# Performance work log

Hardware: AMD Instinct MI355X
Metric: run time of the kernel (lower is better)

Reference implementation:

```python
import jax, jax.numpy as jnp
import numpy as np

BLOCK_Q = 64
BLOCK_KV = 64
TOPK_RATIO = 0.125


def setup_inputs() -> dict:
    key = jax.random.key(0)
    k1, k2, k3 = jax.random.split(key, 3)
    B, H, L, D = 1, 16, 8192, 64
    q = jax.random.normal(k1, (B, H, L, D), dtype=jnp.float32)
    k = jax.random.normal(k2, (B, H, L, D), dtype=jnp.float32)
    v = jax.random.normal(k3, (B, H, L, D), dtype=jnp.float32)
    return {"q": q, "k": k, "v": v}


def _sparse_lut(q, k):
    # get_sparse_map: block mean-pool q and mean-centered k, score blocks, top-k key blocks
    B, H, L, D = q.shape
    Mb, Nb = L // BLOCK_Q, L // BLOCK_KV
    q_pool = q.reshape(B, H, Mb, BLOCK_Q, D).mean(axis=3)          # [B,H,Mb,D]
    smooth_k = k - k.mean(axis=-2, keepdims=True)
    k_pool = smooth_k.reshape(B, H, Nb, BLOCK_KV, D).mean(axis=3)  # [B,H,Nb,D]
    pred = jnp.einsum('bhmd,bhnd->bhmn', q_pool, k_pool)           # [B,H,Mb,Nb]
    topk = int(TOPK_RATIO * Nb)
    _, lut = jax.lax.top_k(pred, topk)                             # [B,H,Mb,topk]
    return lut


def reference(q, k, v):
    B, H, L, D = q.shape
    Mb, Nb = L // BLOCK_Q, L // BLOCK_KV
    lut = _sparse_lut(q, k)                                        # [B,H,Mb,T] int32
    T = lut.shape[-1]
    sm_scale = D ** -0.5

    kb = k.reshape(B, H, Nb, BLOCK_KV, D)
    vb = v.reshape(B, H, Nb, BLOCK_KV, D)
    bi = jnp.arange(B)[:, None, None, None]
    hi = jnp.arange(H)[None, :, None, None]
    # gather selected KV blocks per query block: [B,H,Mb,T,BLOCK_KV,D]
    k_sel = kb[bi, hi, lut].reshape(B, H, Mb, T * BLOCK_KV, D)
    v_sel = vb[bi, hi, lut].reshape(B, H, Mb, T * BLOCK_KV, D)

    qb = q.reshape(B, H, Mb, BLOCK_Q, D)
    s = jnp.einsum('bhmqd,bhmkd->bhmqk', qb, k_sel) * sm_scale     # [B,H,Mb,BQ,T*BKV]
    p = jax.nn.softmax(s, axis=-1)
    o = jnp.einsum('bhmqk,bhmkd->bhmqd', p, v_sel)
    return o.reshape(B, H, L, D)
```

## Files before the change

### kernel.cpp

```cpp
#include <hip/hip_runtime.h>
#include <hip/hip_bf16.h>


#define H_  16
#define L_  8192
#define D_  64
#define MB_ 128
#define NB_ 128
#define TK_ 16
#define ST_ 72

typedef __bf16 bf16x8 __attribute__((ext_vector_type(8)));
typedef __bf16 bf16x4 __attribute__((ext_vector_type(4)));
typedef short  s16x4  __attribute__((ext_vector_type(4)));
typedef float  f32x4  __attribute__((ext_vector_type(4)));
typedef unsigned short u16x8 __attribute__((ext_vector_type(8)));

union BFU { __hip_bfloat16 h; unsigned short u; };

static __device__ inline unsigned short f2bfu(float f) {
  BFU c; c.h = __float2bfloat16(f); return c.u;
}

static __device__ inline f32x4 mfma16(bf16x4 a, bf16x4 b, f32x4 c) {
#if __has_builtin(__builtin_amdgcn_mfma_f32_16x16x16bf16_1k)
  return __builtin_amdgcn_mfma_f32_16x16x16bf16_1k(
      __builtin_bit_cast(s16x4, a), __builtin_bit_cast(s16x4, b), c, 0, 0, 0);
#elif __has_builtin(__builtin_amdgcn_mfma_f32_16x16x16_bf16)
  return __builtin_amdgcn_mfma_f32_16x16x16_bf16(a, b, c, 0, 0, 0);
#else
  f32x4 d = c;
  asm("v_mfma_f32_16x16x16_bf16 %0, %1, %2, %0" : "+v"(d) : "v"(a), "v"(b));
  return d;
#endif
}

static __device__ inline bf16x4 lo4(bf16x8 v) {
  return __builtin_shufflevector(v, v, 0, 1, 2, 3);
}
static __device__ inline bf16x4 hi4(bf16x8 v) {
  return __builtin_shufflevector(v, v, 4, 5, 6, 7);
}

__device__ unsigned short g_qb[(size_t)H_ * L_ * D_];
__device__ unsigned short g_kf[(size_t)H_ * NB_ * 4096];
__device__ unsigned short g_vf[(size_t)H_ * NB_ * 4096];
__device__ float g_qpool[H_ * NB_ * 64];
__device__ float g_kpool[H_ * NB_ * 64];
__device__ int   g_lut[H_ * MB_ * TK_];

static __device__ inline void cvt8_2(const float4& f0, const float4& f1,
                                     unsigned short* dst) {
  u16x8 s;
  s[0] = f2bfu(f0.x); s[1] = f2bfu(f0.y); s[2] = f2bfu(f0.z); s[3] = f2bfu(f0.w);
  s[4] = f2bfu(f1.x); s[5] = f2bfu(f1.y); s[6] = f2bfu(f1.z); s[7] = f2bfu(f1.w);
  *(u16x8*)dst = s;
}

static __device__ inline void cvt8_2s(const float4& f0, const float4& f1,
                                      unsigned short* dst, float sc) {
  u16x8 s;
  s[0] = f2bfu(f0.x * sc); s[1] = f2bfu(f0.y * sc);
  s[2] = f2bfu(f0.z * sc); s[3] = f2bfu(f0.w * sc);
  s[4] = f2bfu(f1.x * sc); s[5] = f2bfu(f1.y * sc);
  s[6] = f2bfu(f1.z * sc); s[7] = f2bfu(f1.w * sc);
  *(u16x8*)dst = s;
}

__global__ __launch_bounds__(256)
void fusedpool_kernel(const float* __restrict__ q,
                      const float* __restrict__ k,
                      const float* __restrict__ v) {
  __shared__ float qt[64 * 64];
  __shared__ float kt[64 * 64];
  __shared__ __align__(16) unsigned short vt_s[64 * ST_];
  __shared__ float pq[4][64], pk[4][64];

  const int b = blockIdx.x;
  const int t = threadIdx.x;
  const int r = t >> 2, c = (t & 3) * 16;
  const size_t base = (size_t)b * 4096 + r * 64 + c;
  const float cs = 0.18033688011112042f;

  float4 qf0 = *(const float4*)(q + base),      qf1 = *(const float4*)(q + base + 4);
  float4 qf2 = *(const float4*)(q + base + 8),  qf3 = *(const float4*)(q + base + 12);
  float4 kf0 = *(const float4*)(k + base),      kf1 = *(const float4*)(k + base + 4);
  float4 kf2 = *(const float4*)(k + base + 8),  kf3 = *(const float4*)(k + base + 12);
  float4 vf0 = *(const float4*)(v + base),      vf1 = *(const float4*)(v + base + 4);
  float4 vf2 = *(const float4*)(v + base + 8),  vf3 = *(const float4*)(v + base + 12);

  cvt8_2s(qf0, qf1, g_qb + base, cs);  cvt8_2s(qf2, qf3, g_qb + base + 8, cs);

  {
    const int w_k = r >> 4, l16k = r & 15;
    const int hf = c >> 5, quadA = (c & 31) >> 3;
    unsigned short* kfp = g_kf + ((size_t)b * 4 + w_k) * 1024 + hf * 512 + l16k * 8;
    cvt8_2(kf0, kf1, kfp + quadA * 128);
    cvt8_2(kf2, kf3, kfp + (quadA + 1) * 128);
  }

  cvt8_2(vf0, vf1, vt_s + r * ST_ + c);
  cvt8_2(vf2, vf3, vt_s + r * ST_ + c + 8);

  *(float4*)(qt + r * 64 + c)      = qf0; *(float4*)(qt + r * 64 + c + 4)  = qf1;
  *(float4*)(qt + r * 64 + c + 8)  = qf2; *(float4*)(qt + r * 64 + c + 12) = qf3;
  *(float4*)(kt + r * 64 + c)      = kf0; *(float4*)(kt + r * 64 + c + 4)  = kf1;
  *(float4*)(kt + r * 64 + c + 8)  = kf2; *(float4*)(kt + r * 64 + c + 12) = kf3;
  __syncthreads();

  const int col = t & 63, g = t >> 6;
  float sq = 0.f, sk = 0.f;
  for (int rr = g * 16; rr < g * 16 + 16; ++rr) {
    sq += qt[rr * 64 + col];
    sk += kt[rr * 64 + col];
  }
  pq[g][col] = sq; pk[g][col] = sk;

  {
    const int wv = t >> 6, lv = t & 63;
    const int l16v = lv & 15, quadv = lv >> 4;
    u16x8 f0, f1;
    #pragma unroll
    for (int n4 = 0; n4 < 2; ++n4)
      #pragma unroll
      for (int rr = 0; rr < 4; ++rr)
        f0[n4 * 4 + rr] = vt_s[(16 * wv + quadv * 4 + rr) * ST_ + 16 * n4 + l16v];
    #pragma unroll
    for (int n4 = 2; n4 < 4; ++n4)
      #pragma unroll
      for (int rr = 0; rr < 4; ++rr)
        f1[(n4 - 2) * 4 + rr] = vt_s[(16 * wv + quadv * 4 + rr) * ST_ + 16 * n4 + l16v];
    unsigned short* vfp = g_vf + ((size_t)b * 4 + wv) * 1024 + lv * 16;
    *(u16x8*)(vfp)     = f0;
    *(u16x8*)(vfp + 8) = f1;
  }

  __syncthreads();
  if (t < 64) {
    g_qpool[b * 64 + t] = (pq[0][t] + pq[1][t] + pq[2][t] + pq[3][t]) * (1.f / 64.f);
    g_kpool[b * 64 + t] = (pk[0][t] + pk[1][t] + pk[2][t] + pk[3][t]) * (1.f / 64.f);
  }
}


__global__ void topk_kernel() {
  const int b = blockIdx.x;
  const int h = b >> 7;
  const int lane = threadIdx.x;
  const float4* qrow = (const float4*)(g_qpool + b * 64);
  const float4* k0 = (const float4*)(g_kpool + (h * NB_ + lane) * 64);
  const float4* k1 = (const float4*)(g_kpool + (h * NB_ + lane + 64) * 64);
  float v0 = 0.f, v1 = 0.f;
  for (int i = 0; i < 16; ++i) {
    float4 qv = qrow[i];
    float4 a = k0[i];
    float4 c = k1[i];
    v0 += qv.x * a.x + qv.y * a.y + qv.z * a.z + qv.w * a.w;
    v1 += qv.x * c.x + qv.y * c.y + qv.z * c.z + qv.w * c.w;
  }
  for (int t = 0; t < TK_; ++t) {
    float bv; int bi;
    if (v0 >= v1) { bv = v0; bi = lane; } else { bv = v1; bi = lane + 64; }
    for (int mask = 1; mask < 64; mask <<= 1) {
      float ov = __shfl_xor(bv, mask, 64);
      int   oi = __shfl_xor(bi, mask, 64);
      if (ov > bv || (ov == bv && oi < bi)) { bv = ov; bi = oi; }
    }
    if (lane == 0) g_lut[b * TK_ + t] = bi;
    if (bi == lane) v0 = -3.0e38f;
    else if (bi == lane + 64) v1 = -3.0e38f;
  }
}

__global__ __launch_bounds__(256, 3)
void attn_kernel(float* __restrict__ out) {
  __shared__ float LDSo[4][16][65];
  __shared__ float LDSr[4][64];

  const int flat = blockIdx.x;
  const int h = (flat & 7) * 2 + ((flat >> 10) & 1);
  const int m = (flat >> 3) & 127;
  const int t = threadIdx.x;
  const int w = t >> 6;
  const int lane = t & 63;
  const int l16 = lane & 15, quad = lane >> 4;

  const unsigned short* qg = g_qb + ((size_t)h * L_ + (size_t)m * 64) * D_;
  bf16x8 qb0[4], qb1[4];
  #pragma unroll
  for (int g = 0; g < 4; ++g) {
    const unsigned short* qp = qg + (16 * g + l16) * 64 + quad * 8;
    qb0[g] = *(const bf16x8*)(qp);
    qb1[g] = *(const bf16x8*)(qp + 32);
  }

  f32x4 o[4][4];
  #pragma unroll
  for (int n4 = 0; n4 < 4; ++n4)
    #pragma unroll
    for (int g = 0; g < 4; ++g) o[n4][g] = (f32x4){0.f, 0.f, 0.f, 0.f};
  float lsum[4] = {0.f, 0.f, 0.f, 0.f};

  const int* my_lut = g_lut + (h * MB_ + m) * TK_;

  bf16x8 ka0[2], ka1[2], vv01[2], vv23[2];

  {
    const int kb0 = __builtin_amdgcn_readfirstlane(my_lut[0]);
    const unsigned short* kbp = g_kf + ((size_t)(h * NB_ + kb0) * 4 + w) * 1024;
    ka0[0] = *(const bf16x8*)(kbp + lane * 8);
    ka1[0] = *(const bf16x8*)(kbp + 512 + lane * 8);
    const unsigned short* vbp = g_vf + ((size_t)(h * NB_ + kb0) * 4 + w) * 1024 + lane * 16;
    vv01[0] = *(const bf16x8*)(vbp);
    vv23[0] = *(const bf16x8*)(vbp + 8);
  }

  #pragma unroll
  for (int j = 0; j < TK_; ++j) {
    const int cb = j & 1, nb = cb ^ 1;
    if (j + 1 < TK_) {
      const int kbn = __builtin_amdgcn_readfirstlane(my_lut[j + 1]);
      const unsigned short* kbp = g_kf + ((size_t)(h * NB_ + kbn) * 4 + w) * 1024;
      ka0[nb] = *(const bf16x8*)(kbp + lane * 8);
      ka1[nb] = *(const bf16x8*)(kbp + 512 + lane * 8);
      const unsigned short* vbp = g_vf + ((size_t)(h * NB_ + kbn) * 4 + w) * 1024 + lane * 16;
      vv01[nb] = *(const bf16x8*)(vbp);
      vv23[nb] = *(const bf16x8*)(vbp + 8);
    }

    f32x4 acc[4];
    __builtin_amdgcn_s_setprio(1);
    #pragma unroll
    for (int g = 0; g < 4; ++g) {
      f32x4 z = (f32x4){0.f, 0.f, 0.f, 0.f};
      z = __builtin_amdgcn_mfma_f32_16x16x32_bf16(ka0[cb], qb0[g], z, 0, 0, 0);
      z = __builtin_amdgcn_mfma_f32_16x16x32_bf16(ka1[cb], qb1[g], z, 0, 0, 0);
      acc[g] = z;
    }
    __builtin_amdgcn_s_setprio(0);

    bf16x4 pb[4];
    #pragma unroll
    for (int g = 0; g < 4; ++g) {
      const float p0 = exp2f(acc[g][0]), p1 = exp2f(acc[g][1]);
      const float p2 = exp2f(acc[g][2]), p3 = exp2f(acc[g][3]);
      lsum[g] += (p0 + p1) + (p2 + p3);
      unsigned int d0, d1;
      asm("v_cvt_pk_bf16_f32 %0, %1, %2" : "=v"(d0) : "v"(p0), "v"(p1));
      asm("v_cvt_pk_bf16_f32 %0, %1, %2" : "=v"(d1) : "v"(p2), "v"(p3));
      uint2 dd; dd.x = d0; dd.y = d1;
      pb[g] = __builtin_bit_cast(bf16x4, dd);
    }

    const bf16x4 va_[4] = { lo4(vv01[cb]), hi4(vv01[cb]),
                            lo4(vv23[cb]), hi4(vv23[cb]) };
    __builtin_amdgcn_s_setprio(1);
    #pragma unroll
    for (int n4 = 0; n4 < 4; ++n4)
      #pragma unroll
      for (int g = 0; g < 4; ++g)
        o[n4][g] = mfma16(va_[n4], pb[g], o[n4][g]);
    __builtin_amdgcn_s_setprio(0);
  }

  #pragma unroll
  for (int g = 0; g < 4; ++g) {
    float rs = lsum[g];
    rs += __shfl_xor(rs, 16, 64);
    rs += __shfl_xor(rs, 32, 64);
    lsum[g] = rs;
  }
  if (quad == 0) {
    #pragma unroll
    for (int g = 0; g < 4; ++g) LDSr[w][16 * g + l16] = lsum[g];
  }
  __syncthreads();

  const int dr = t & 15, q0 = (t >> 4) * 4;
  float rinv[4];
  #pragma unroll
  for (int qq = 0; qq < 4; ++qq)
    rinv[qq] = 1.0f / (LDSr[0][q0 + qq] + LDSr[1][q0 + qq] +
                       LDSr[2][q0 + qq] + LDSr[3][q0 + qq]);

  const size_t obase = ((size_t)h * L_ + (size_t)m * 64) * D_;
  #pragma unroll
  for (int n4 = 0; n4 < 4; ++n4) {
    #pragma unroll
    for (int g = 0; g < 4; ++g)
      #pragma unroll
      for (int r = 0; r < 4; ++r)
        LDSo[w][quad * 4 + r][16 * g + l16] = o[n4][g][r];
    __syncthreads();
    #pragma unroll
    for (int qq = 0; qq < 4; ++qq) {
      const int qv = q0 + qq;
      const float s = LDSo[0][dr][qv] + LDSo[1][dr][qv] +
                      LDSo[2][dr][qv] + LDSo[3][dr][qv];
      out[obase + (size_t)qv * 64 + n4 * 16 + dr] = s * rinv[qq];
    }
    __syncthreads();
  }
}

extern "C" void kernel_launch(void* const* d_in, const int* in_sizes, int n_in,
                              void* d_out, int out_size, void* d_ws, size_t ws_size,
                              hipStream_t stream) {
  const float* q = (const float*)d_in[0];
  const float* k = (const float*)d_in[1];
  const float* v = (const float*)d_in[2];
  float* out = (float*)d_out;

  fusedpool_kernel<<<H_ * NB_, 256, 0, stream>>>(q, k, v);
  topk_kernel<<<H_ * MB_, 64, 0, stream>>>();
  attn_kernel<<<H_ * MB_, 256, 0, stream>>>(out);
}
```

Baseline: 221.5 us.

## Fuse top-k selection into attention kernel and split query rows across 8 waves

The separate top-k kernel is removed. Wave 0 of each attention block now computes the block scores and top-k indices into shared memory, and the whole block synchronises before the attention loop starts. The block grows to 512 threads so that two wave groups each handle 32 of the 64 query rows, while four waves split the KV block as before. This saves one kernel launch and the global LUT round trip, but the other waves idle while wave 0 runs the serial top-k, and K/V fragments are now loaded twice per block.

```diff
diff --git a/kernel.cpp b/kernel.cpp
--- a/kernel.cpp
+++ b/kernel.cpp
@@ -47,7 +47,6 @@
 __device__ unsigned short g_vf[(size_t)H_ * NB_ * 4096];
 __device__ float g_qpool[H_ * NB_ * 64];
 __device__ float g_kpool[H_ * NB_ * 64];
-__device__ int   g_lut[H_ * MB_ * TK_];
 
 static __device__ inline void cvt8_2(const float4& f0, const float4& f1,
                                      unsigned short* dst) {
@@ -143,74 +142,76 @@
 }
 
 
-__global__ void topk_kernel() {
-  const int b = blockIdx.x;
-  const int h = b >> 7;
-  const int lane = threadIdx.x;
-  const float4* qrow = (const float4*)(g_qpool + b * 64);
-  const float4* k0 = (const float4*)(g_kpool + (h * NB_ + lane) * 64);
-  const float4* k1 = (const float4*)(g_kpool + (h * NB_ + lane + 64) * 64);
-  float v0 = 0.f, v1 = 0.f;
-  for (int i = 0; i < 16; ++i) {
-    float4 qv = qrow[i];
-    float4 a = k0[i];
-    float4 c = k1[i];
-    v0 += qv.x * a.x + qv.y * a.y + qv.z * a.z + qv.w * a.w;
-    v1 += qv.x * c.x + qv.y * c.y + qv.z * c.z + qv.w * c.w;
-  }
-  for (int t = 0; t < TK_; ++t) {
-    float bv; int bi;
-    if (v0 >= v1) { bv = v0; bi = lane; } else { bv = v1; bi = lane + 64; }
-    for (int mask = 1; mask < 64; mask <<= 1) {
-      float ov = __shfl_xor(bv, mask, 64);
-      int   oi = __shfl_xor(bi, mask, 64);
-      if (ov > bv || (ov == bv && oi < bi)) { bv = ov; bi = oi; }
-    }
-    if (lane == 0) g_lut[b * TK_ + t] = bi;
-    if (bi == lane) v0 = -3.0e38f;
-    else if (bi == lane + 64) v1 = -3.0e38f;
-  }
-}
-
-__global__ __launch_bounds__(256, 3)
+__global__ __launch_bounds__(512, 4)
 void attn_kernel(float* __restrict__ out) {
-  __shared__ float LDSo[4][16][65];
-  __shared__ float LDSr[4][64];
+  __shared__ float LDSo[8][16][33];
+  __shared__ float LDSr[8][32];
+  __shared__ int   ls_lut[TK_];
 
   const int flat = blockIdx.x;
   const int h = (flat & 7) * 2 + ((flat >> 10) & 1);
   const int m = (flat >> 3) & 127;
   const int t = threadIdx.x;
   const int w = t >> 6;
+  const int wq = w >> 2, wkv = w & 3;
   const int lane = t & 63;
   const int l16 = lane & 15, quad = lane >> 4;
 
   const unsigned short* qg = g_qb + ((size_t)h * L_ + (size_t)m * 64) * D_;
-  bf16x8 qb0[4], qb1[4];
-  #pragma unroll
-  for (int g = 0; g < 4; ++g) {
-    const unsigned short* qp = qg + (16 * g + l16) * 64 + quad * 8;
+  bf16x8 qb0[2], qb1[2];
+  #pragma unroll
+  for (int g = 0; g < 2; ++g) {
+    const unsigned short* qp = qg + (32 * wq + 16 * g + l16) * 64 + quad * 8;
     qb0[g] = *(const bf16x8*)(qp);
     qb1[g] = *(const bf16x8*)(qp + 32);
   }
 
-  f32x4 o[4][4];
+  if (w == 0) {
+    const int b = h * MB_ + m;
+    const float4* qrow = (const float4*)(g_qpool + b * 64);
+    const float4* k0 = (const float4*)(g_kpool + (h * NB_ + lane) * 64);
+    const float4* k1 = (const float4*)(g_kpool + (h * NB_ + lane + 64) * 64);
+    float v0 = 0.f, v1 = 0.f;
+    for (int i = 0; i < 16; ++i) {
+      float4 qv = qrow[i];
+      float4 a = k0[i];
+      float4 c = k1[i];
+      v0 += qv.x * a.x + qv.y * a.y + qv.z * a.z + qv.w * a.w;
+      v1 += qv.x * c.x + qv.y * c.y + qv.z * c.z + qv.w * c.w;
+    }
+    for (int tt = 0; tt < TK_; ++tt) {
+      float bv; int bi;
+      if (v0 >= v1) { bv = v0; bi = lane; } else { bv = v1; bi = lane + 64; }
+      for (int mask = 1; mask < 64; mask <<= 1) {
+        float ov = __shfl_xor(bv, mask, 64);
+        int   oi = __shfl_xor(bi, mask, 64);
+        if (ov > bv || (ov == bv && oi < bi)) { bv = ov; bi = oi; }
+      }
+      if (lane == 0) ls_lut[tt] = bi;
+      if (bi == lane) v0 = -3.0e38f;
+      else if (bi == lane + 64) v1 = -3.0e38f;
+    }
+  }
+  __syncthreads();
+
+  f32x4 o[4][2];
   #pragma unroll
   for (int n4 = 0; n4 < 4; ++n4)
     #pragma unroll
-    for (int g = 0; g < 4; ++g) o[n4][g] = (f32x4){0.f, 0.f, 0.f, 0.f};
-  float lsum[4] = {0.f, 0.f, 0.f, 0.f};
-
-  const int* my_lut = g_lut + (h * MB_ + m) * TK_;
+    for (int g = 0; g < 2; ++g) o[n4][g] = (f32x4){0.f, 0.f, 0.f, 0.f};
+  float lsum[2] = {0.f, 0.f};
+
+  const unsigned short* kfh = g_kf + (size_t)h * NB_ * 4096;
+  const unsigned short* vfh = g_vf + (size_t)h * NB_ * 4096;
 
   bf16x8 ka0[2], ka1[2], vv01[2], vv23[2];
 
   {
-    const int kb0 = __builtin_amdgcn_readfirstlane(my_lut[0]);
-    const unsigned short* kbp = g_kf + ((size_t)(h * NB_ + kb0) * 4 + w) * 1024;
+    const int kb0 = __builtin_amdgcn_readfirstlane(ls_lut[0]);
+    const unsigned short* kbp = kfh + ((size_t)kb0 * 4 + wkv) * 1024;
     ka0[0] = *(const bf16x8*)(kbp + lane * 8);
     ka1[0] = *(const bf16x8*)(kbp + 512 + lane * 8);
-    const unsigned short* vbp = g_vf + ((size_t)(h * NB_ + kb0) * 4 + w) * 1024 + lane * 16;
+    const unsigned short* vbp = vfh + ((size_t)kb0 * 4 + wkv) * 1024 + lane * 16;
     vv01[0] = *(const bf16x8*)(vbp);
     vv23[0] = *(const bf16x8*)(vbp + 8);
   }
@@ -219,19 +220,19 @@
   for (int j = 0; j < TK_; ++j) {
     const int cb = j & 1, nb = cb ^ 1;
     if (j + 1 < TK_) {
-      const int kbn = __builtin_amdgcn_readfirstlane(my_lut[j + 1]);
-      const unsigned short* kbp = g_kf + ((size_t)(h * NB_ + kbn) * 4 + w) * 1024;
+      const int kbn = __builtin_amdgcn_readfirstlane(ls_lut[j + 1]);
+      const unsigned short* kbp = kfh + ((size_t)kbn * 4 + wkv) * 1024;
       ka0[nb] = *(const bf16x8*)(kbp + lane * 8);
       ka1[nb] = *(const bf16x8*)(kbp + 512 + lane * 8);
-      const unsigned short* vbp = g_vf + ((size_t)(h * NB_ + kbn) * 4 + w) * 1024 + lane * 16;
+      const unsigned short* vbp = vfh + ((size_t)kbn * 4 + wkv) * 1024 + lane * 16;
       vv01[nb] = *(const bf16x8*)(vbp);
       vv23[nb] = *(const bf16x8*)(vbp + 8);
     }
 
-    f32x4 acc[4];
+    f32x4 acc[2];
     __builtin_amdgcn_s_setprio(1);
     #pragma unroll
-    for (int g = 0; g < 4; ++g) {
+    for (int g = 0; g < 2; ++g) {
       f32x4 z = (f32x4){0.f, 0.f, 0.f, 0.f};
       z = __builtin_amdgcn_mfma_f32_16x16x32_bf16(ka0[cb], qb0[g], z, 0, 0, 0);
       z = __builtin_amdgcn_mfma_f32_16x16x32_bf16(ka1[cb], qb1[g], z, 0, 0, 0);
@@ -239,9 +240,9 @@
     }
     __builtin_amdgcn_s_setprio(0);
 
-    bf16x4 pb[4];
-    #pragma unroll
-    for (int g = 0; g < 4; ++g) {
+    bf16x4 pb[2];
+    #pragma unroll
+    for (int g = 0; g < 2; ++g) {
       const float p0 = exp2f(acc[g][0]), p1 = exp2f(acc[g][1]);
       const float p2 = exp2f(acc[g][2]), p3 = exp2f(acc[g][3]);
       lsum[g] += (p0 + p1) + (p2 + p3);
@@ -258,13 +259,13 @@
     #pragma unroll
     for (int n4 = 0; n4 < 4; ++n4)
       #pragma unroll
-      for (int g = 0; g < 4; ++g)
+      for (int g = 0; g < 2; ++g)
         o[n4][g] = mfma16(va_[n4], pb[g], o[n4][g]);
     __builtin_amdgcn_s_setprio(0);
   }
 
   #pragma unroll
-  for (int g = 0; g < 4; ++g) {
+  for (int g = 0; g < 2; ++g) {
     float rs = lsum[g];
     rs += __shfl_xor(rs, 16, 64);
     rs += __shfl_xor(rs, 32, 64);
@@ -272,32 +273,32 @@
   }
   if (quad == 0) {
     #pragma unroll
-    for (int g = 0; g < 4; ++g) LDSr[w][16 * g + l16] = lsum[g];
+    for (int g = 0; g < 2; ++g) LDSr[w][16 * g + l16] = lsum[g];
   }
   __syncthreads();
 
-  const int dr = t & 15, q0 = (t >> 4) * 4;
-  float rinv[4];
-  #pragma unroll
-  for (int qq = 0; qq < 4; ++qq)
-    rinv[qq] = 1.0f / (LDSr[0][q0 + qq] + LDSr[1][q0 + qq] +
-                       LDSr[2][q0 + qq] + LDSr[3][q0 + qq]);
+  const int dr = t & 15, qi = t >> 4;
+  float rinv[2];
+  #pragma unroll
+  for (int pr = 0; pr < 2; ++pr)
+    rinv[pr] = 1.0f / (LDSr[pr * 4 + 0][qi] + LDSr[pr * 4 + 1][qi] +
+                       LDSr[pr * 4 + 2][qi] + LDSr[pr * 4 + 3][qi]);
 
   const size_t obase = ((size_t)h * L_ + (size_t)m * 64) * D_;
   #pragma unroll
   for (int n4 = 0; n4 < 4; ++n4) {
     #pragma unroll
-    for (int g = 0; g < 4; ++g)
+    for (int g = 0; g < 2; ++g)
       #pragma unroll
       for (int r = 0; r < 4; ++r)
         LDSo[w][quad * 4 + r][16 * g + l16] = o[n4][g][r];
     __syncthreads();
     #pragma unroll
-    for (int qq = 0; qq < 4; ++qq) {
-      const int qv = q0 + qq;
-      const float s = LDSo[0][dr][qv] + LDSo[1][dr][qv] +
-                      LDSo[2][dr][qv] + LDSo[3][dr][qv];
-      out[obase + (size_t)qv * 64 + n4 * 16 + dr] = s * rinv[qq];
+    for (int pr = 0; pr < 2; ++pr) {
+      const int qv = qi + 32 * pr;
+      const float s = LDSo[pr * 4 + 0][dr][qi] + LDSo[pr * 4 + 1][dr][qi] +
+                      LDSo[pr * 4 + 2][dr][qi] + LDSo[pr * 4 + 3][dr][qi];
+      out[obase + (size_t)qv * 64 + n4 * 16 + dr] = s * rinv[pr];
     }
     __syncthreads();
   }
@@ -312,6 +313,5 @@
   float* out = (float*)d_out;
 
   fusedpool_kernel<<<H_ * NB_, 256, 0, stream>>>(q, k, v);
-  topk_kernel<<<H_ * MB_, 64, 0, stream>>>();
-  attn_kernel<<<H_ * MB_, 256, 0, stream>>>(out);
-}
+  attn_kernel<<<H_ * MB_, 512, 0, stream>>>(out);
+}
```

Measured after the change: 246.2 us. 11.1% more time.
